# Performance work log

Measured on AMD Instinct MI355X. Metric: run time of the kernel, lower is better.

## Reference

```python
import jax, jax.numpy as jnp
import numpy as np

MAX_DELAY = 441      # int(10.0/1000*44100 + 0.5)
FEEDBACK = 0.5
WIDTH = 1.0
DEPTH = 1.0
MIX = 0.7


def setup_inputs() -> dict:
    key = jax.random.key(0)
    k1, k2 = jax.random.split(key)
    x = jax.random.normal(k1, (8, 2, 32768), dtype=jnp.float32)
    mod_sig = jax.random.uniform(k2, (8, 2, 32768), dtype=jnp.float32)  # LFO in [0,1]
    return {"x": x, "mod_sig": mod_sig}


def _flanger(x, mod_sig):
    # x, mod_sig: [B, C, N]; circular delay line of length D with fractional read
    B, C, N = x.shape
    D = MAX_DELAY
    buf0 = jnp.zeros((B, C, D), dtype=x.dtype)
    widxs = jnp.arange(N, dtype=jnp.int32) % D  # circular write index per step

    def step(buf, inp):
        audio, mod, widx = inp                       # audio, mod: [B, C]
        delay = (D * WIDTH) * mod                    # fractional delay in samples
        read = (widx.astype(x.dtype) - delay + D) % D
        prev = jnp.floor(read)
        frac = read - prev                           # linear-interp fraction
        pi = prev.astype(jnp.int32)
        ni = (pi + 1) % D
        prev_val = jnp.take_along_axis(buf, pi[..., None], axis=-1)[..., 0]
        next_val = jnp.take_along_axis(buf, ni[..., None], axis=-1)[..., 0]
        interp = frac * next_val + (1.0 - frac) * prev_val
        buf = buf.at[:, :, widx].set(audio + FEEDBACK * interp)  # feedback write
        return buf, audio + DEPTH * interp

    xs = (jnp.moveaxis(x, -1, 0), jnp.moveaxis(mod_sig, -1, 0), widxs)
    _, out = jax.lax.scan(step, buf0, xs)            # out: [N, B, C]
    out = jnp.moveaxis(out, 0, -1)                   # [B, C, N]
    return (1.0 - MIX) * x + MIX * out


def reference(x, mod_sig):
    return _flanger(x, mod_sig)
```

## Files before the change

### kernel.cpp

```cpp
#include <hip/hip_runtime.h>


#define NSAMP  32768
#define DLY    441
#define CHUNK  512
#define HALO   2816
#define WLEN   (CHUNK + HALO)
#define JN     (WLEN / 256)
#define JKEEP  (HALO / 256)
#define SWEEPS 6
#define ZSLOT  WLEN

__global__ __launch_bounds__(256, 4) void flanger_fused(
    const float* __restrict__ x, const float* __restrict__ mod,
    float* __restrict__ out)
{
    __shared__ float V[2][WLEN + 1];

    const int t   = threadIdx.x;
    const int blk = blockIdx.x;
    const int ch  = blk >> 6;
    const int ck  = blk & 63;
    const int g0  = ck * CHUNK;
    const int wg0 = g0 - HALO;

    const float* xc = x   + ch * NSAMP;
    const float* mc = mod + ch * NSAMP;

    float xr[JN], gr[JN];
    int   ta[JN], tb[JN];

    int w = ((wg0 + t) % DLY + DLY) % DLY;

    #pragma unroll
    for (int j = 0; j < JN; ++j) {
        const int nl = t + 256 * j;
        const int gn = wg0 + nl;
        if (gn >= 0) {
            const float xv = xc[gn];
            const float m  = mc[gn];
            xr[j] = xv;
            const float delay = 441.0f * m;
            float read = (float)w - delay;
            if (read < 0.0f) read += 441.0f;
            const float pf = floorf(read);
            gr[j] = read - pf;
            const int pi = (int)pf;
            int ni = pi + 1; if (ni == DLY) ni = 0;
            int da = w - pi; if (da <= 0) da += DLY;
            int db = w - ni; if (db <= 0) db += DLY;
            int a = nl - da; if (a < 0) a = ZSLOT;
            int b = nl - db; if (b < 0) b = ZSLOT;
            ta[j] = a;
            tb[j] = b;
            V[0][nl] = xv;
        } else {
            xr[j] = 0.0f; gr[j] = 0.0f;
            ta[j] = ZSLOT; tb[j] = ZSLOT;
            V[0][nl] = 0.0f;
        }
        w += 256; if (w >= DLY) w -= DLY;
    }
    if (t == 0) { V[0][ZSLOT] = 0.0f; V[1][ZSLOT] = 0.0f; }
    __syncthreads();

    #pragma unroll
    for (int i = 1; i <= SWEEPS; ++i) {
        const int lo   = HALO - (SWEEPS - i + 1) * 442;
        const int jmin = (lo <= 0) ? 0 : (lo >> 8);
        const float* __restrict__ Vo = V[(i + 1) & 1];
        float* __restrict__       Vn = V[i & 1];
        #pragma unroll
        for (int j = 0; j < JN; ++j) {
            if (j >= jmin) {
                const float vp = Vo[ta[j]];
                const float vn = Vo[tb[j]];
                const float y  = gr[j] * vn + (1.0f - gr[j]) * vp;
                Vn[t + 256 * j] = xr[j] + 0.5f * y;
            }
        }
        __syncthreads();
    }

    const float* __restrict__ Vf = V[SWEEPS & 1];
    float* o = out + ch * NSAMP + g0;
    #pragma unroll
    for (int j = JKEEP; j < JN; ++j) {
        const float vp = Vf[ta[j]];
        const float vn = Vf[tb[j]];
        const float y  = gr[j] * vn + (1.0f - gr[j]) * vp;
        o[t + 256 * (j - JKEEP)] = xr[j] + 0.7f * y;
    }
}

extern "C" void kernel_launch(void* const* d_in, const int* in_sizes, int n_in,
                              void* d_out, int out_size, void* d_ws, size_t ws_size,
                              hipStream_t stream) {
    const float* x   = (const float*)d_in[0];
    const float* mod = (const float*)d_in[1];
    float*       out = (float*)d_out;

    dim3 grid(1024), block(256);
    flanger_fused<<<grid, block, 0, stream>>>(x, mod, out);
}
```

Before: 67.91 us.

## Double chunk size to 1024 with 512 threads and use adjacent-slot interpolation reads

Each block now handles a 1024-sample chunk with 512 threads and a 3072-sample halo, so the share of redundant halo work per output sample drops. The interpolation now reads the next tap as the adjacent shared-memory slot (ta+1), which the compiler can fuse into a paired LDS load. Wraparound and zero-slot cases are flagged per element and patched on a rarely taken branch. This halves the grid and doubles block size, which may reduce occupancy and add branch divergence where rare cases occur.

```diff
diff --git a/kernel.cpp b/kernel.cpp
--- a/kernel.cpp
+++ b/kernel.cpp
@@ -3,24 +3,25 @@
 
 #define NSAMP  32768
 #define DLY    441
-#define CHUNK  512
-#define HALO   2816
+#define NTHR   512
+#define CHUNK  1024
+#define HALO   3072
 #define WLEN   (CHUNK + HALO)
-#define JN     (WLEN / 256)
-#define JKEEP  (HALO / 256)
+#define JN     (WLEN / NTHR)
+#define JKEEP  (HALO / NTHR)
 #define SWEEPS 6
 #define ZSLOT  WLEN
 
-__global__ __launch_bounds__(256, 4) void flanger_fused(
+__global__ __launch_bounds__(NTHR, 2) void flanger_fused(
     const float* __restrict__ x, const float* __restrict__ mod,
     float* __restrict__ out)
 {
-    __shared__ float V[2][WLEN + 1];
+    __shared__ float V[2][WLEN + 2];
 
     const int t   = threadIdx.x;
     const int blk = blockIdx.x;
-    const int ch  = blk >> 6;
-    const int ck  = blk & 63;
+    const int ch  = blk >> 5;
+    const int ck  = blk & 31;
     const int g0  = ck * CHUNK;
     const int wg0 = g0 - HALO;
 
@@ -28,13 +29,13 @@
     const float* mc = mod + ch * NSAMP;
 
     float xr[JN], gr[JN];
-    int   ta[JN], tb[JN];
+    int   ta[JN], tb[JN], rr[JN];
 
     int w = ((wg0 + t) % DLY + DLY) % DLY;
 
     #pragma unroll
     for (int j = 0; j < JN; ++j) {
-        const int nl = t + 256 * j;
+        const int nl = t + NTHR * j;
         const int gn = wg0 + nl;
         if (gn >= 0) {
             const float xv = xc[gn];
@@ -49,34 +50,49 @@
             int ni = pi + 1; if (ni == DLY) ni = 0;
             int da = w - pi; if (da <= 0) da += DLY;
             int db = w - ni; if (db <= 0) db += DLY;
-            int a = nl - da; if (a < 0) a = ZSLOT;
-            int b = nl - db; if (b < 0) b = ZSLOT;
-            ta[j] = a;
-            tb[j] = b;
+            const int ta_raw = nl - da;
+            const int tb_raw = nl - db;
+            int rare = (da == 1) | ((ta_raw < 0) & (tb_raw >= 0));
+            ta[j] = (ta_raw < 0) ? ZSLOT : ta_raw;
+            tb[j] = (tb_raw < 0) ? ZSLOT : tb_raw;
+            rr[j] = rare;
             V[0][nl] = xv;
         } else {
             xr[j] = 0.0f; gr[j] = 0.0f;
-            ta[j] = ZSLOT; tb[j] = ZSLOT;
+            ta[j] = ZSLOT; tb[j] = ZSLOT; rr[j] = 0;
             V[0][nl] = 0.0f;
         }
-        w += 256; if (w >= DLY) w -= DLY;
+        w += NTHR;
+        if (w >= DLY) w -= DLY;
+        if (w >= DLY) w -= DLY;
     }
-    if (t == 0) { V[0][ZSLOT] = 0.0f; V[1][ZSLOT] = 0.0f; }
+    if (t == 0) {
+        V[0][ZSLOT] = 0.0f; V[0][ZSLOT + 1] = 0.0f;
+        V[1][ZSLOT] = 0.0f; V[1][ZSLOT + 1] = 0.0f;
+    }
     __syncthreads();
 
     #pragma unroll
     for (int i = 1; i <= SWEEPS; ++i) {
         const int lo   = HALO - (SWEEPS - i + 1) * 442;
-        const int jmin = (lo <= 0) ? 0 : (lo >> 8);
+        const int jmin = (lo <= 0) ? 0 : (lo / NTHR);
         const float* __restrict__ Vo = V[(i + 1) & 1];
         float* __restrict__       Vn = V[i & 1];
         #pragma unroll
         for (int j = 0; j < JN; ++j) {
             if (j >= jmin) {
+                const float g  = gr[j];
                 const float vp = Vo[ta[j]];
-                const float vn = Vo[tb[j]];
-                const float y  = gr[j] * vn + (1.0f - gr[j]) * vp;
-                Vn[t + 256 * j] = xr[j] + 0.5f * y;
+                const float vn = Vo[ta[j] + 1];
+                const float y  = g * vn + (1.0f - g) * vp;
+                Vn[t + NTHR * j] = xr[j] + 0.5f * y;
+                if (rr[j]) {
+                    int tbj = tb[j];
+                    asm volatile("" : "+v"(tbj));
+                    const float vn2 = Vo[tbj];
+                    const float y2  = g * vn2 + (1.0f - g) * vp;
+                    Vn[t + NTHR * j] = xr[j] + 0.5f * y2;
+                }
             }
         }
         __syncthreads();
@@ -86,10 +102,16 @@
     float* o = out + ch * NSAMP + g0;
     #pragma unroll
     for (int j = JKEEP; j < JN; ++j) {
+        const float g  = gr[j];
         const float vp = Vf[ta[j]];
-        const float vn = Vf[tb[j]];
-        const float y  = gr[j] * vn + (1.0f - gr[j]) * vp;
-        o[t + 256 * (j - JKEEP)] = xr[j] + 0.7f * y;
+        float       vn = Vf[ta[j] + 1];
+        if (rr[j]) {
+            int tbj = tb[j];
+            asm volatile("" : "+v"(tbj));
+            vn = Vf[tbj];
+        }
+        const float y = g * vn + (1.0f - g) * vp;
+        o[t + NTHR * (j - JKEEP)] = xr[j] + 0.7f * y;
     }
 }
 
@@ -100,6 +122,6 @@
     const float* mod = (const float*)d_in[1];
     float*       out = (float*)d_out;
 
-    dim3 grid(1024), block(256);
+    dim3 grid(512), block(NTHR);
     flanger_fused<<<grid, block, 0, stream>>>(x, mod, out);
 }
```

New measurement: 64.81 us. -4.6%, faster.
